# Performance work log

Measured on AMD Instinct MI355X. Metric: run time of the kernel, lower is better.

Reference implementation:

```python
import jax, jax.numpy as jnp
import numpy as np

C = 32
H = 8

def _layernorm(x, scale, bias, eps=1e-5):
    mu = jnp.mean(x, axis=-1, keepdims=True)
    var = jnp.mean(jnp.square(x - mu), axis=-1, keepdims=True)
    return (x - mu) * jax.lax.rsqrt(var + eps) * scale + bias


def setup_inputs() -> dict:
    key = jax.random.key(0)
    ks = jax.random.split(key, 10)
    B, s, i, j = 1, 128, 256, 256
    m = jax.random.normal(ks[0], (B, s, i, C), dtype=jnp.float32)
    z = jax.random.normal(ks[1], (B, i, j, C), dtype=jnp.float32)
    sd = 1.0 / np.sqrt(C)
    return {
        "m": m,
        "z": z,
        "ln_scale": jnp.ones((C,), jnp.float32),
        "ln_bias": jnp.zeros((C,), jnp.float32),
        "lnb_scale": jnp.ones((C,), jnp.float32),
        "lnb_bias": jnp.zeros((C,), jnp.float32),
        "wq": jax.random.normal(ks[2], (C, C * H), jnp.float32) * sd,
        "wk": jax.random.normal(ks[3], (C, C * H), jnp.float32) * sd,
        "wv": jax.random.normal(ks[4], (C, C * H), jnp.float32) * sd,
        "wb": jax.random.normal(ks[5], (C, H), jnp.float32) * sd,
        "wg": jax.random.normal(ks[6], (C, C * H), jnp.float32) * sd,
        "wo": jax.random.normal(ks[7], (C * H, C), jnp.float32) * (1.0 / np.sqrt(C * H)),
        "bo": jnp.zeros((C,), jnp.float32),
    }


def reference(m, z, ln_scale, ln_bias, lnb_scale, lnb_bias, wq, wk, wv, wb, wg, wo, bo):
    B, s, i, _ = m.shape
    j = z.shape[2]
    mn = _layernorm(m, ln_scale, ln_bias)                      # (B,s,i,c)
    q = (mn @ wq).reshape(B, s, i, H, C)                        # (B,s,i,h,c)
    k = (mn @ wk).reshape(B, s, i, H, C)
    v = (mn @ wv).reshape(B, s, i, H, C)
    gate = jax.nn.sigmoid(mn @ wg).reshape(B, s, i, H, C)       # (B,s,i,h,c)
    b = (_layernorm(z, lnb_scale, lnb_bias) @ wb)               # (B,i,j,h)
    a = jnp.einsum('bsihc,bsjhc->bsijh', q, k) * (C ** -0.5) + b[:, None]
    a = jax.nn.softmax(a, axis=-2)                              # softmax over j
    o = gate * jnp.einsum('bsijh,bsjhc->bsihc', a, v)
    o = o.reshape(B, s, i, H * C)
    return o @ wo + bo
```

## Files before the change

### kernel.cpp

```cpp
#include <hip/hip_runtime.h>

constexpr int NC = 32;
constexpr int NH = 8;
constexpr int NS = 128;
constexpr int NI = 256;
constexpr int NJ = 256;
constexpr float LN_EPS = 1e-5f;
constexpr float QSCALE = 0.17677669529663687f;
constexpr float LOG2E  = 1.4426950408889634f;

typedef __bf16 bf16x8 __attribute__((ext_vector_type(8)));
typedef __bf16 bf16x2 __attribute__((ext_vector_type(2)));
typedef float floatx4 __attribute__((ext_vector_type(4)));

__device__ __forceinline__ float fexp2(float x) {
#if __has_builtin(__builtin_amdgcn_exp2f)
    return __builtin_amdgcn_exp2f(x);
#else
    return exp2f(x);
#endif
}
__device__ __forceinline__ float frcp(float x) {
#if __has_builtin(__builtin_amdgcn_rcpf)
    return __builtin_amdgcn_rcpf(x);
#else
    return 1.0f / x;
#endif
}
__device__ __forceinline__ unsigned pk2c(float a, float b) {
    union { bf16x2 v; unsigned u; } c;
    c.v = bf16x2{(__bf16)a, (__bf16)b};
    return c.u;
}
__device__ __forceinline__ unsigned pkbb(__bf16 a, __bf16 b) {
    union { bf16x2 v; unsigned u; } c;
    c.v = bf16x2{a, b};
    return c.u;
}

__device__ __forceinline__ int qkOff(int row, int chunk) {
    return row * 32 + ((chunk ^ ((row >> 1) & 3)) << 3);
}
__device__ __forceinline__ int vOff(int c, int chunk) {
    return c * 256 + ((chunk ^ (c & 7)) << 3);
}

__global__ __launch_bounds__(256) void biasprep_kernel(
    const float* __restrict__ z, const float* __restrict__ lnb_s,
    const float* __restrict__ lnb_b, const float* __restrict__ wb,
    const float* __restrict__ wq, const float* __restrict__ wk,
    const float* __restrict__ wv, const float* __restrict__ wg,
    const float* __restrict__ wo,
    float* __restrict__ bias32, unsigned short* __restrict__ wprep,
    unsigned short* __restrict__ wofrag)
{
    const int b = blockIdx.x;
    const int t = threadIdx.x;
    if (b < 256) {
        __shared__ float zL[256 * 33];
        const float4* src = (const float4*)(z + (size_t)b * NJ * NC);
#pragma unroll
        for (int k = 0; k < 8; ++k) {
            int idx = t + 256 * k;
            float4 v = src[idx];
            int f = idx * 4;
            int j = f >> 5, c = f & 31;
            zL[j * 33 + c]     = v.x; zL[j * 33 + c + 1] = v.y;
            zL[j * 33 + c + 2] = v.z; zL[j * 33 + c + 3] = v.w;
        }
        __syncthreads();

        float x[NC];
#pragma unroll
        for (int c = 0; c < NC; ++c) x[c] = zL[t * 33 + c];
        float mu = 0.f;
#pragma unroll
        for (int c = 0; c < NC; ++c) mu += x[c];
        mu *= (1.0f / NC);
        float var = 0.f;
#pragma unroll
        for (int c = 0; c < NC; ++c) { float d = x[c] - mu; var += d * d; }
        var *= (1.0f / NC);
        float rs = rsqrtf(var + LN_EPS);
        float acc[NH];
#pragma unroll
        for (int h = 0; h < NH; ++h) acc[h] = 0.f;
#pragma unroll
        for (int c = 0; c < NC; ++c) {
            float xn = (x[c] - mu) * rs * lnb_s[c] + lnb_b[c];
#pragma unroll
            for (int h = 0; h < NH; ++h) acc[h] += xn * wb[c * NH + h];
        }
        const int i = b;
        const int w_ = i >> 6, it = (i >> 4) & 3, lm = i & 15;
        const int jc = t >> 5, jt = (t >> 4) & 1, lq = (t >> 2) & 3, r = t & 3;
        const int base = jc * 8192 + w_ * 2048 + (jt * 4 + it) * 256
                       + (lq * 16 + lm) * 4 + r;
#pragma unroll
        for (int h = 0; h < NH; ++h)
            bias32[h * 65536 + base] = acc[h] * LOG2E;
    } else if (b < 272) {
        int g = (b - 256) * 256 + t;
        int p  = g >> 10;
        int h  = (g >> 7) & 7;
        int ct = (g >> 6) & 1;
        int l  = g & 63;
        const float* W = (p == 0) ? wq : (p == 1) ? wk : (p == 2) ? wv : wg;
        float scale = (p == 0) ? QSCALE * LOG2E : (p == 3) ? LOG2E : 1.0f;
        int col = 32 * h + 16 * ct + (l & 15);
        int r0  = 8 * (l >> 4);
        float v[8];
#pragma unroll
        for (int e = 0; e < 8; ++e) v[e] = W[(r0 + e) * 256 + col] * scale;
        uint4 u;
        u.x = pk2c(v[0], v[1]); u.y = pk2c(v[2], v[3]);
        u.z = pk2c(v[4], v[5]); u.w = pk2c(v[6], v[7]);
        *(uint4*)&wprep[g * 8] = u;
    } else {
        int g = (b - 272) * 256 + t;
        int tile = g >> 6;
        int l = g & 63;
        int kt = tile >> 1, nt = tile & 1;
        int r0 = kt * 32 + 8 * (l >> 4);
        int col = nt * 16 + (l & 15);
        float v[8];
#pragma unroll
        for (int e = 0; e < 8; ++e) v[e] = wo[(r0 + e) * 32 + col];
        uint4 u;
        u.x = pk2c(v[0], v[1]); u.y = pk2c(v[2], v[3]);
        u.z = pk2c(v[4], v[5]); u.w = pk2c(v[6], v[7]);
        *(uint4*)&wofrag[g * 8] = u;
    }
}

__global__ __launch_bounds__(256, 3) void attn_kernel(
    const float* __restrict__ m, const float* __restrict__ ln_s,
    const float* __restrict__ ln_b,
    const unsigned short* __restrict__ wprep,
    const float* __restrict__ bias32,
    unsigned short* __restrict__ attn16)
{
    __shared__ unsigned short QPX[256 * 32];
    __shared__ unsigned short Kt[256 * 32];
    __shared__ unsigned short Vt[32 * 256];

    const int t = threadIdx.x;
    const int h = blockIdx.x & 7;
    const int s = blockIdx.x >> 3;
    const int l = t & 63, w = t >> 6;
    const int lm = l & 15, lq = l >> 4;
    const int ibase = w * 64;
    const floatx4 zero = {0.f, 0.f, 0.f, 0.f};

    {
        const float4* mr = (const float4*)(m + ((size_t)s * NI + t) * NC);
        float x[NC];
#pragma unroll
        for (int k = 0; k < 8; ++k) {
            float4 v = mr[k];
            x[4*k] = v.x; x[4*k+1] = v.y; x[4*k+2] = v.z; x[4*k+3] = v.w;
        }
        float mu = 0.f;
#pragma unroll
        for (int c = 0; c < NC; ++c) mu += x[c];
        mu *= (1.0f / NC);
        float var = 0.f;
#pragma unroll
        for (int c = 0; c < NC; ++c) { float d = x[c] - mu; var += d * d; }
        var *= (1.0f / NC);
        float rs = rsqrtf(var + LN_EPS);
#pragma unroll
        for (int k = 0; k < 4; ++k) {
            uint4 u;
            u.x = pk2c((x[8*k+0]-mu)*rs*ln_s[8*k+0]+ln_b[8*k+0],
                       (x[8*k+1]-mu)*rs*ln_s[8*k+1]+ln_b[8*k+1]);
            u.y = pk2c((x[8*k+2]-mu)*rs*ln_s[8*k+2]+ln_b[8*k+2],
                       (x[8*k+3]-mu)*rs*ln_s[8*k+3]+ln_b[8*k+3]);
            u.z = pk2c((x[8*k+4]-mu)*rs*ln_s[8*k+4]+ln_b[8*k+4],
                       (x[8*k+5]-mu)*rs*ln_s[8*k+5]+ln_b[8*k+5]);
            u.w = pk2c((x[8*k+6]-mu)*rs*ln_s[8*k+6]+ln_b[8*k+6],
                       (x[8*k+7]-mu)*rs*ln_s[8*k+7]+ln_b[8*k+7]);
            *(uint4*)&QPX[qkOff(t, k)] = u;
        }
    }

    const unsigned short* wp = wprep + ((size_t)h * 128 + l) * 8;
    bf16x8 wfQ[2], wfK[2], wfV[2];
#pragma unroll
    for (int ct = 0; ct < 2; ++ct) {
        wfQ[ct] = *(const bf16x8*)&wp[(0 * 1024 + ct * 64) * 8];
        wfK[ct] = *(const bf16x8*)&wp[(1 * 1024 + ct * 64) * 8];
        wfV[ct] = *(const bf16x8*)&wp[(2 * 1024 + ct * 64) * 8];
    }
    bf16x8 Xb[4];
#pragma unroll
    for (int it = 0; it < 4; ++it)
        Xb[it] = *(const bf16x8*)&QPX[qkOff(ibase + it * 16 + lm, lq)];

#pragma unroll
    for (int it = 0; it < 4; ++it)
#pragma unroll
        for (int ct = 0; ct < 2; ++ct) {
            floatx4 d = __builtin_amdgcn_mfma_f32_16x16x32_bf16(wfQ[ct], Xb[it], zero, 0, 0, 0);
            uint2 u; u.x = pk2c(d[0], d[1]); u.y = pk2c(d[2], d[3]);
            int row = ibase + it * 16 + lm;
            *(uint2*)&QPX[qkOff(row, 2 * ct + (lq >> 1)) + (lq & 1) * 4] = u;
        }
#pragma unroll
    for (int it = 0; it < 4; ++it)
#pragma unroll
        for (int ct = 0; ct < 2; ++ct) {
            floatx4 d = __builtin_amdgcn_mfma_f32_16x16x32_bf16(wfK[ct], Xb[it], zero, 0, 0, 0);
            uint2 u; u.x = pk2c(d[0], d[1]); u.y = pk2c(d[2], d[3]);
            int row = ibase + it * 16 + lm;
            *(uint2*)&Kt[qkOff(row, 2 * ct + (lq >> 1)) + (lq & 1) * 4] = u;
        }
#pragma unroll
    for (int jt = 0; jt < 4; ++jt)
#pragma unroll
        for (int ct = 0; ct < 2; ++ct) {
            floatx4 d = __builtin_amdgcn_mfma_f32_16x16x32_bf16(Xb[jt], wfV[ct], zero, 0, 0, 0);
            uint2 u; u.x = pk2c(d[0], d[1]); u.y = pk2c(d[2], d[3]);
            int c = ct * 16 + lm;
            int chunk = 8 * w + 2 * jt + (lq >> 1);
            *(uint2*)&Vt[vOff(c, chunk) + (lq & 1) * 4] = u;
        }

    bf16x8 Qb[4];
#pragma unroll
    for (int it = 0; it < 4; ++it)
        Qb[it] = *(const bf16x8*)&QPX[qkOff(ibase + it * 16 + lm, lq)];

    __syncthreads();

    floatx4 accO[2][4];
#pragma unroll
    for (int ct = 0; ct < 2; ++ct)
#pragma unroll
        for (int it = 0; it < 4; ++it) accO[ct][it] = zero;
    floatx4 accL[4];
#pragma unroll
    for (int it = 0; it < 4; ++it) accL[it] = zero;
    bf16x8 ones;
#pragma unroll
    for (int e = 0; e < 8; ++e) ones[e] = (__bf16)1.0f;

    const float* bptr = bias32 + (size_t)h * 65536 + w * 2048 + l * 4;

    for (int jc = 0; jc < 8; ++jc) {
        const int j0 = jc * 32;
        const float* bj = bptr + jc * 8192;

#pragma unroll
        for (int jt = 0; jt < 2; ++jt) {
            bf16x8 Ka = *(const bf16x8*)&Kt[qkOff(j0 + jt * 16 + lm, lq)];
#pragma unroll
            for (int it = 0; it < 4; ++it) {
                floatx4 C = *(const floatx4*)(bj + (jt * 4 + it) * 256);
                floatx4 S = __builtin_amdgcn_mfma_f32_16x16x32_bf16(Ka, Qb[it], C, 0, 0, 0);
                __bf16 p0 = (__bf16)fexp2(S[0]);
                __bf16 p1 = (__bf16)fexp2(S[1]);
                __bf16 p2 = (__bf16)fexp2(S[2]);
                __bf16 p3 = (__bf16)fexp2(S[3]);
                uint2 u; u.x = pkbb(p0, p1); u.y = pkbb(p2, p3);
                int row = ibase + it * 16 + lm;
                *(uint2*)&QPX[qkOff(row, 2 * jt + (lq >> 1)) + (lq & 1) * 4] = u;
            }
        }

        bf16x8 Va0 = *(const bf16x8*)&Vt[vOff(lm, 4 * jc + lq)];
        bf16x8 Va1 = *(const bf16x8*)&Vt[vOff(16 + lm, 4 * jc + lq)];
#pragma unroll
        for (int it = 0; it < 4; ++it) {
            bf16x8 Pb = *(const bf16x8*)&QPX[qkOff(ibase + it * 16 + lm, lq)];
            accO[0][it] = __builtin_amdgcn_mfma_f32_16x16x32_bf16(Va0, Pb, accO[0][it], 0, 0, 0);
            accO[1][it] = __builtin_amdgcn_mfma_f32_16x16x32_bf16(Va1, Pb, accO[1][it], 0, 0, 0);
            accL[it]    = __builtin_amdgcn_mfma_f32_16x16x32_bf16(ones, Pb, accL[it], 0, 0, 0);
        }
    }

    float gt[2][4][4];
    {
        bf16x8 wfG0 = *(const bf16x8*)&wp[(3 * 1024 + 0 * 64) * 8];
        bf16x8 wfG1 = *(const bf16x8*)&wp[(3 * 1024 + 1 * 64) * 8];
#pragma unroll
        for (int it = 0; it < 4; ++it) {
            floatx4 d0 = __builtin_amdgcn_mfma_f32_16x16x32_bf16(wfG0, Xb[it], zero, 0, 0, 0);
            floatx4 d1 = __builtin_amdgcn_mfma_f32_16x16x32_bf16(wfG1, Xb[it], zero, 0, 0, 0);
#pragma unroll
            for (int r = 0; r < 4; ++r) {
                gt[0][it][r] = frcp(1.0f + fexp2(-d0[r]));
                gt[1][it][r] = frcp(1.0f + fexp2(-d1[r]));
            }
        }
    }
#pragma unroll
    for (int it = 0; it < 4; ++it) {
        const float inv = frcp(accL[it][0]);
        const size_t rowb = ((size_t)s * NI + ibase + it * 16 + lm) * 256 + h * 32;
#pragma unroll
        for (int ct = 0; ct < 2; ++ct) {
            float o0 = accO[ct][it][0] * inv * gt[ct][it][0];
            float o1 = accO[ct][it][1] * inv * gt[ct][it][1];
            float o2 = accO[ct][it][2] * inv * gt[ct][it][2];
            float o3 = accO[ct][it][3] * inv * gt[ct][it][3];
            uint2 u; u.x = pk2c(o0, o1); u.y = pk2c(o2, o3);
            *(uint2*)&attn16[rowb + ct * 16 + lq * 4] = u;
        }
    }
}

__global__ __launch_bounds__(256) void proj_kernel(
    const unsigned short* __restrict__ attn16,
    const unsigned short* __restrict__ wofrag,
    const float* __restrict__ bo, float* __restrict__ out)
{
    const int t = threadIdx.x;
    const int l = t & 63, w = t >> 6;
    const int lm = l & 15, lq = l >> 4;
    const int row0 = blockIdx.x * 128 + w * 32;
    const floatx4 zero = {0.f, 0.f, 0.f, 0.f};

    floatx4 acc[2][2];
#pragma unroll
    for (int it = 0; it < 2; ++it)
#pragma unroll
        for (int nt = 0; nt < 2; ++nt) acc[it][nt] = zero;

#pragma unroll 2
    for (int kt = 0; kt < 8; ++kt) {
        bf16x8 a0 = *(const bf16x8*)&attn16[(size_t)(row0 + lm) * 256 + kt * 32 + lq * 8];
        bf16x8 a1 = *(const bf16x8*)&attn16[(size_t)(row0 + 16 + lm) * 256 + kt * 32 + lq * 8];
        bf16x8 b0 = *(const bf16x8*)&wofrag[((kt * 2 + 0) * 64 + l) * 8];
        bf16x8 b1 = *(const bf16x8*)&wofrag[((kt * 2 + 1) * 64 + l) * 8];
        acc[0][0] = __builtin_amdgcn_mfma_f32_16x16x32_bf16(a0, b0, acc[0][0], 0, 0, 0);
        acc[0][1] = __builtin_amdgcn_mfma_f32_16x16x32_bf16(a0, b1, acc[0][1], 0, 0, 0);
        acc[1][0] = __builtin_amdgcn_mfma_f32_16x16x32_bf16(a1, b0, acc[1][0], 0, 0, 0);
        acc[1][1] = __builtin_amdgcn_mfma_f32_16x16x32_bf16(a1, b1, acc[1][1], 0, 0, 0);
    }

    float bov[2] = {bo[lm], bo[16 + lm]};
#pragma unroll
    for (int it = 0; it < 2; ++it)
#pragma unroll
        for (int nt = 0; nt < 2; ++nt)
#pragma unroll
            for (int r = 0; r < 4; ++r)
                out[(size_t)(row0 + it * 16 + lq * 4 + r) * NC + nt * 16 + lm]
                    = acc[it][nt][r] + bov[nt];
}

extern "C" void kernel_launch(void* const* d_in, const int* in_sizes, int n_in,
                              void* d_out, int out_size, void* d_ws, size_t ws_size,
                              hipStream_t stream) {
    const float* m     = (const float*)d_in[0];
    const float* z     = (const float*)d_in[1];
    const float* ln_s  = (const float*)d_in[2];
    const float* ln_b  = (const float*)d_in[3];
    const float* lnb_s = (const float*)d_in[4];
    const float* lnb_b = (const float*)d_in[5];
    const float* wq    = (const float*)d_in[6];
    const float* wk    = (const float*)d_in[7];
    const float* wv    = (const float*)d_in[8];
    const float* wb    = (const float*)d_in[9];
    const float* wg    = (const float*)d_in[10];
    const float* wo    = (const float*)d_in[11];
    const float* bo    = (const float*)d_in[12];
    float* out = (float*)d_out;

    float* bias32 = (float*)d_ws;
    unsigned short* wprep  = (unsigned short*)((char*)d_ws + (2u << 20));
    unsigned short* wofrag = (unsigned short*)((char*)d_ws + (2u << 20) + 65536);
    unsigned short* attn16 = (unsigned short*)((char*)d_ws + (2u << 20) + 65536 + 16384);

    biasprep_kernel<<<276, 256, 0, stream>>>(z, lnb_s, lnb_b, wb, wq, wk, wv, wg,
                                             wo, bias32, wprep, wofrag);
    attn_kernel<<<NS * NH, 256, 0, stream>>>(m, ln_s, ln_b, wprep, bias32, attn16);
    proj_kernel<<<(NS * NI) / 128, 256, 0, stream>>>(attn16, wofrag, bo, out);
}
```

Baseline: 120.2 us.

## Shrink attention LDS footprint and replace ones-MFMA row sums with shuffles

The attention kernel drops the 16KB QPX buffer and stages the LN output and Q in the K buffer instead, which is later overwritten by K. The probability tile now goes through a smaller 8KB Ps buffer, processed in two halves per j-chunk. The extra MFMA that multiplied by a ones vector to get softmax denominators is replaced by scalar accumulation plus cross-lane shuffles. Launch bounds rise from 3 to 4 blocks per CU. The goal is to cut LDS use and MFMA work so more blocks fit per CU, at the cost of more register pressure and tighter ordering between shared-memory reuse phases.

```diff
diff --git a/kernel.cpp b/kernel.cpp
--- a/kernel.cpp
+++ b/kernel.cpp
@@ -133,16 +133,16 @@
     }
 }
 
-__global__ __launch_bounds__(256, 3) void attn_kernel(
+__global__ __launch_bounds__(256, 4) void attn_kernel(
     const float* __restrict__ m, const float* __restrict__ ln_s,
     const float* __restrict__ ln_b,
     const unsigned short* __restrict__ wprep,
     const float* __restrict__ bias32,
     unsigned short* __restrict__ attn16)
 {
-    __shared__ unsigned short QPX[256 * 32];
     __shared__ unsigned short Kt[256 * 32];
     __shared__ unsigned short Vt[32 * 256];
+    __shared__ unsigned short Ps[128 * 32];
 
     const int t = threadIdx.x;
     const int h = blockIdx.x & 7;
@@ -180,7 +180,7 @@
                        (x[8*k+5]-mu)*rs*ln_s[8*k+5]+ln_b[8*k+5]);
             u.w = pk2c((x[8*k+6]-mu)*rs*ln_s[8*k+6]+ln_b[8*k+6],
                        (x[8*k+7]-mu)*rs*ln_s[8*k+7]+ln_b[8*k+7]);
-            *(uint4*)&QPX[qkOff(t, k)] = u;
+            *(uint4*)&Kt[qkOff(t, k)] = u;
         }
     }
 
@@ -195,7 +195,7 @@
     bf16x8 Xb[4];
 #pragma unroll
     for (int it = 0; it < 4; ++it)
-        Xb[it] = *(const bf16x8*)&QPX[qkOff(ibase + it * 16 + lm, lq)];
+        Xb[it] = *(const bf16x8*)&Kt[qkOff(ibase + it * 16 + lm, lq)];
 
 #pragma unroll
     for (int it = 0; it < 4; ++it)
@@ -204,8 +204,13 @@
             floatx4 d = __builtin_amdgcn_mfma_f32_16x16x32_bf16(wfQ[ct], Xb[it], zero, 0, 0, 0);
             uint2 u; u.x = pk2c(d[0], d[1]); u.y = pk2c(d[2], d[3]);
             int row = ibase + it * 16 + lm;
-            *(uint2*)&QPX[qkOff(row, 2 * ct + (lq >> 1)) + (lq & 1) * 4] = u;
-        }
+            *(uint2*)&Kt[qkOff(row, 2 * ct + (lq >> 1)) + (lq & 1) * 4] = u;
+        }
+    bf16x8 Qb[4];
+#pragma unroll
+    for (int it = 0; it < 4; ++it)
+        Qb[it] = *(const bf16x8*)&Kt[qkOff(ibase + it * 16 + lm, lq)];
+
 #pragma unroll
     for (int it = 0; it < 4; ++it)
 #pragma unroll
@@ -226,11 +231,6 @@
             *(uint2*)&Vt[vOff(c, chunk) + (lq & 1) * 4] = u;
         }
 
-    bf16x8 Qb[4];
-#pragma unroll
-    for (int it = 0; it < 4; ++it)
-        Qb[it] = *(const bf16x8*)&QPX[qkOff(ibase + it * 16 + lm, lq)];
-
     __syncthreads();
 
     floatx4 accO[2][4];
@@ -238,44 +238,45 @@
     for (int ct = 0; ct < 2; ++ct)
 #pragma unroll
         for (int it = 0; it < 4; ++it) accO[ct][it] = zero;
-    floatx4 accL[4];
-#pragma unroll
-    for (int it = 0; it < 4; ++it) accL[it] = zero;
-    bf16x8 ones;
-#pragma unroll
-    for (int e = 0; e < 8; ++e) ones[e] = (__bf16)1.0f;
+    float lsum[4] = {0.f, 0.f, 0.f, 0.f};
 
     const float* bptr = bias32 + (size_t)h * 65536 + w * 2048 + l * 4;
 
     for (int jc = 0; jc < 8; ++jc) {
         const int j0 = jc * 32;
         const float* bj = bptr + jc * 8192;
-
-#pragma unroll
-        for (int jt = 0; jt < 2; ++jt) {
-            bf16x8 Ka = *(const bf16x8*)&Kt[qkOff(j0 + jt * 16 + lm, lq)];
-#pragma unroll
-            for (int it = 0; it < 4; ++it) {
-                floatx4 C = *(const floatx4*)(bj + (jt * 4 + it) * 256);
-                floatx4 S = __builtin_amdgcn_mfma_f32_16x16x32_bf16(Ka, Qb[it], C, 0, 0, 0);
-                __bf16 p0 = (__bf16)fexp2(S[0]);
-                __bf16 p1 = (__bf16)fexp2(S[1]);
-                __bf16 p2 = (__bf16)fexp2(S[2]);
-                __bf16 p3 = (__bf16)fexp2(S[3]);
-                uint2 u; u.x = pkbb(p0, p1); u.y = pkbb(p2, p3);
-                int row = ibase + it * 16 + lm;
-                *(uint2*)&QPX[qkOff(row, 2 * jt + (lq >> 1)) + (lq & 1) * 4] = u;
-            }
-        }
-
+        bf16x8 Ka0 = *(const bf16x8*)&Kt[qkOff(j0 + lm, lq)];
+        bf16x8 Ka1 = *(const bf16x8*)&Kt[qkOff(j0 + 16 + lm, lq)];
         bf16x8 Va0 = *(const bf16x8*)&Vt[vOff(lm, 4 * jc + lq)];
         bf16x8 Va1 = *(const bf16x8*)&Vt[vOff(16 + lm, 4 * jc + lq)];
-#pragma unroll
-        for (int it = 0; it < 4; ++it) {
-            bf16x8 Pb = *(const bf16x8*)&QPX[qkOff(ibase + it * 16 + lm, lq)];
-            accO[0][it] = __builtin_amdgcn_mfma_f32_16x16x32_bf16(Va0, Pb, accO[0][it], 0, 0, 0);
-            accO[1][it] = __builtin_amdgcn_mfma_f32_16x16x32_bf16(Va1, Pb, accO[1][it], 0, 0, 0);
-            accL[it]    = __builtin_amdgcn_mfma_f32_16x16x32_bf16(ones, Pb, accL[it], 0, 0, 0);
+
+#pragma unroll
+        for (int half = 0; half < 2; ++half) {
+#pragma unroll
+            for (int jt = 0; jt < 2; ++jt) {
+                bf16x8 Ka = jt ? Ka1 : Ka0;
+#pragma unroll
+                for (int q = 0; q < 2; ++q) {
+                    int it = half * 2 + q;
+                    floatx4 C = *(const floatx4*)(bj + (jt * 4 + it) * 256);
+                    floatx4 S = __builtin_amdgcn_mfma_f32_16x16x32_bf16(Ka, Qb[it], C, 0, 0, 0);
+                    __bf16 p0 = (__bf16)fexp2(S[0]);
+                    __bf16 p1 = (__bf16)fexp2(S[1]);
+                    __bf16 p2 = (__bf16)fexp2(S[2]);
+                    __bf16 p3 = (__bf16)fexp2(S[3]);
+                    lsum[it] += ((float)p0 + (float)p1) + ((float)p2 + (float)p3);
+                    uint2 u; u.x = pkbb(p0, p1); u.y = pkbb(p2, p3);
+                    int row = w * 32 + q * 16 + lm;
+                    *(uint2*)&Ps[qkOff(row, 2 * jt + (lq >> 1)) + (lq & 1) * 4] = u;
+                }
+            }
+#pragma unroll
+            for (int q = 0; q < 2; ++q) {
+                int it = half * 2 + q;
+                bf16x8 Pb = *(const bf16x8*)&Ps[qkOff(w * 32 + q * 16 + lm, lq)];
+                accO[0][it] = __builtin_amdgcn_mfma_f32_16x16x32_bf16(Va0, Pb, accO[0][it], 0, 0, 0);
+                accO[1][it] = __builtin_amdgcn_mfma_f32_16x16x32_bf16(Va1, Pb, accO[1][it], 0, 0, 0);
+            }
         }
     }
 
@@ -294,16 +295,23 @@
             }
         }
     }
+    float inv[4];
 #pragma unroll
     for (int it = 0; it < 4; ++it) {
-        const float inv = frcp(accL[it][0]);
+        float v = lsum[it];
+        v += __shfl_xor(v, 16, 64);
+        v += __shfl_xor(v, 32, 64);
+        inv[it] = frcp(v);
+    }
+#pragma unroll
+    for (int it = 0; it < 4; ++it) {
         const size_t rowb = ((size_t)s * NI + ibase + it * 16 + lm) * 256 + h * 32;
 #pragma unroll
         for (int ct = 0; ct < 2; ++ct) {
-            float o0 = accO[ct][it][0] * inv * gt[ct][it][0];
-            float o1 = accO[ct][it][1] * inv * gt[ct][it][1];
-            float o2 = accO[ct][it][2] * inv * gt[ct][it][2];
-            float o3 = accO[ct][it][3] * inv * gt[ct][it][3];
+            float o0 = accO[ct][it][0] * inv[it] * gt[ct][it][0];
+            float o1 = accO[ct][it][1] * inv[it] * gt[ct][it][1];
+            float o2 = accO[ct][it][2] * inv[it] * gt[ct][it][2];
+            float o3 = accO[ct][it][3] * inv[it] * gt[ct][it][3];
             uint2 u; u.x = pk2c(o0, o1); u.y = pk2c(o2, o3);
             *(uint2*)&attn16[rowb + ct * 16 + lq * 4] = u;
         }
```

Result: slower. 129.5 us (+7.8%).
